# Performance work log

Measured on AMD Instinct MI355X. Metric: run time of the kernel, lower is better.

Reference implementation:

```python
import jax, jax.numpy as jnp
import numpy as np

N = 80000      # nodes
E = 1280000    # edges
G = 64         # graphs in batch
CIN = 128
D = 64
NUM_LAYERS = 6


def setup_inputs() -> dict:
    key = jax.random.key(0)
    ks = jax.random.split(key, 12)
    s = 0.05
    return {
        "x": jax.random.normal(ks[0], (N, CIN), jnp.float32),
        "edge_index": jax.random.randint(ks[1], (2, E), 0, N, dtype=jnp.int32),
        "batch": jnp.sort(jax.random.randint(ks[2], (N,), 0, G, dtype=jnp.int32)),
        "W_in": jax.random.normal(ks[3], (CIN, D), jnp.float32) * s,
        "b_in": jnp.zeros((D,), jnp.float32),
        "W_hid": jax.random.normal(ks[4], (NUM_LAYERS - 1, D, D), jnp.float32) * s,
        "b_hid": jnp.zeros((NUM_LAYERS - 1, D), jnp.float32),
        "lin1_w": jax.random.normal(ks[5], (2 * D, 64), jnp.float32) * s,
        "lin1_b": jnp.zeros((64,), jnp.float32),
        "lin2_w": jax.random.normal(ks[6], (64, 64), jnp.float32) * s,
        "lin2_b": jnp.zeros((64,), jnp.float32),
        "lin3_w": jax.random.normal(ks[7], (64, 1), jnp.float32) * s,
        "lin3_b": jnp.zeros((1,), jnp.float32),
    }


def _gcn_norm(edge_index, n):
    # PyG gcn_norm: add self-loops, symmetric D^-1/2 (A+I) D^-1/2 normalization
    loops = jnp.arange(n, dtype=edge_index.dtype)
    src = jnp.concatenate([edge_index[0], loops])
    dst = jnp.concatenate([edge_index[1], loops])
    deg = jax.ops.segment_sum(jnp.ones_like(src, jnp.float32), dst, num_segments=n)
    dinv = jnp.where(deg > 0, jax.lax.rsqrt(jnp.maximum(deg, 1.0)), 0.0)
    norm = dinv[src] * dinv[dst]
    return src, dst, norm


def _gcn_conv(x, W, b, src, dst, norm, n):
    h = x @ W                                   # [N, D]
    msg = h[src] * norm[:, None]                # [E+N, D] gather + scale
    out = jax.ops.segment_sum(msg, dst, num_segments=n)
    return out + b


def reference(x, edge_index, batch, W_in, b_in, W_hid, b_hid,
              lin1_w, lin1_b, lin2_w, lin2_b, lin3_w, lin3_b):
    n = x.shape[0]
    src, dst, norm = _gcn_norm(edge_index, n)
    # layer 0: in_channels -> D, then ReLU
    h = jax.nn.relu(_gcn_conv(x, W_in, b_in, src, dst, norm, n))
    # hidden layers: ReLU on all but the last conv
    n_hid = W_hid.shape[0]
    for i in range(n_hid):
        h = _gcn_conv(h, W_hid[i], b_hid[i], src, dst, norm, n)
        if i != n_hid - 1:
            h = jax.nn.relu(h)
    # global add + max pooling per graph
    x1 = jax.ops.segment_sum(h, batch, num_segments=G)   # [G, D]
    x2 = jax.ops.segment_max(h, batch, num_segments=G)   # [G, D]
    g = jnp.concatenate([x1, x2], axis=1)                # [G, 2D]
    g = jax.nn.relu(g @ lin1_w + lin1_b)
    g = jax.nn.relu(g @ lin2_w + lin2_b)
    return g @ lin3_w + lin3_b                           # [G, 1]
```

## Files before the change

### kernel.cpp

```cpp
#include <hip/hip_runtime.h>
#include <hip/hip_bf16.h>
#include <cstdint>
#include <cstddef>


#define FEAT 64


__global__ __launch_bounds__(256) void init_kernel(int* deg, int* cursor,
    float* gsum, unsigned int* gmax, int n) {
  int i = blockIdx.x * 256 + threadIdx.x;
  if (i < n) { deg[i] = 0; cursor[i] = 0; }
  if (i < 64 * FEAT) { gsum[i] = 0.f; gmax[i] = 0xFF800000u; }
}

__global__ __launch_bounds__(256) void hist_kernel(const int* __restrict__ dst,
    int* __restrict__ deg, int e) {
  int i = blockIdx.x * 256 + threadIdx.x;
  if (i < e) atomicAdd(&deg[dst[i]], 1);
}

__global__ __launch_bounds__(256) void dinv_kernel(const int* __restrict__ deg,
    float* __restrict__ dinv, int n) {
  int i = blockIdx.x * 256 + threadIdx.x;
  if (i < n) dinv[i] = rsqrtf((float)(deg[i] + 1));
}

__global__ __launch_bounds__(256) void scan1_kernel(const int* __restrict__ deg,
    int* __restrict__ offs, int* __restrict__ bsums, int n) {
  __shared__ int buf[256];
  int t = threadIdx.x;
  int i = blockIdx.x * 256 + t;
  int v = (i < n) ? deg[i] : 0;
  buf[t] = v;
  __syncthreads();
  for (int off = 1; off < 256; off <<= 1) {
    int add = (t >= off) ? buf[t - off] : 0;
    __syncthreads();
    buf[t] += add;
    __syncthreads();
  }
  if (i < n) offs[i] = buf[t] - v;
  if (t == 255) bsums[blockIdx.x] = buf[255];
}

__global__ __launch_bounds__(512) void scan2_kernel(int* bs, int nb) {
  __shared__ int buf[512];
  int t = threadIdx.x;
  int v = (t < nb) ? bs[t] : 0;
  buf[t] = v;
  __syncthreads();
  for (int off = 1; off < 512; off <<= 1) {
    int add = (t >= off) ? buf[t - off] : 0;
    __syncthreads();
    buf[t] += add;
    __syncthreads();
  }
  if (t < nb) bs[t] = buf[t] - v;
}

__global__ __launch_bounds__(256) void scan3_kernel(int* __restrict__ offs,
    const int* __restrict__ bs, int n) {
  int i = blockIdx.x * 256 + threadIdx.x;
  if (i < n) offs[i] += bs[blockIdx.x];
}

__global__ __launch_bounds__(256) void fill_kernel(const int* __restrict__ src,
    const int* __restrict__ dst, const int* __restrict__ offs,
    int* __restrict__ cursor, int* __restrict__ csr_src, int e) {
  int i = blockIdx.x * 256 + threadIdx.x;
  if (i >= e) return;
  int d = dst[i], s = src[i];
  int pos = offs[d] + atomicAdd(&cursor[d], 1);
  csr_src[pos] = s;
}

template <int K>
__global__ __launch_bounds__(256, 2) void gemm_kernel(
    const float* __restrict__ in, const float* __restrict__ W,
    const float* __restrict__ dinv, float* __restrict__ out, int n) {
  __shared__ float in_lds[64 * K];
  const int lane = threadIdx.x & 63;
  const int wid = threadIdx.x >> 6;

  float wreg[K];
#pragma unroll
  for (int k = 0; k < K; ++k) wreg[k] = W[k * 64 + lane];

  const int ntiles = n >> 6;
  for (int tile = blockIdx.x; tile < ntiles; tile += gridDim.x) {
    const float* tin = in + (size_t)tile * 64 * K;
    __syncthreads();
#pragma unroll
    for (int i = threadIdx.x; i < 16 * K; i += 256)
      *(float4*)&in_lds[i * 4] = *(const float4*)&tin[i * 4];
    __syncthreads();

    float* tout = out + (size_t)tile * 64 * 64;
    const float* dvp = dinv + tile * 64;
#pragma unroll
    for (int g = 0; g < 4; ++g) {
      const int r0 = wid * 16 + g * 4;
      float a0 = 0.f, a1 = 0.f, a2 = 0.f, a3 = 0.f;
#pragma unroll
      for (int k = 0; k < K; k += 4) {
        float4 x0 = *(const float4*)&in_lds[(r0 + 0) * K + k];
        float4 x1 = *(const float4*)&in_lds[(r0 + 1) * K + k];
        float4 x2 = *(const float4*)&in_lds[(r0 + 2) * K + k];
        float4 x3 = *(const float4*)&in_lds[(r0 + 3) * K + k];
        a0 = fmaf(x0.x, wreg[k + 0], a0); a0 = fmaf(x0.y, wreg[k + 1], a0);
        a0 = fmaf(x0.z, wreg[k + 2], a0); a0 = fmaf(x0.w, wreg[k + 3], a0);
        a1 = fmaf(x1.x, wreg[k + 0], a1); a1 = fmaf(x1.y, wreg[k + 1], a1);
        a1 = fmaf(x1.z, wreg[k + 2], a1); a1 = fmaf(x1.w, wreg[k + 3], a1);
        a2 = fmaf(x2.x, wreg[k + 0], a2); a2 = fmaf(x2.y, wreg[k + 1], a2);
        a2 = fmaf(x2.z, wreg[k + 2], a2); a2 = fmaf(x2.w, wreg[k + 3], a2);
        a3 = fmaf(x3.x, wreg[k + 0], a3); a3 = fmaf(x3.y, wreg[k + 1], a3);
        a3 = fmaf(x3.z, wreg[k + 2], a3); a3 = fmaf(x3.w, wreg[k + 3], a3);
      }
      tout[(r0 + 0) * 64 + lane] = a0 * dvp[r0 + 0];
      tout[(r0 + 1) * 64 + lane] = a1 * dvp[r0 + 1];
      tout[(r0 + 2) * 64 + lane] = a2 * dvp[r0 + 2];
      tout[(r0 + 3) * 64 + lane] = a3 * dvp[r0 + 3];
    }
  }
}

__global__ __launch_bounds__(256) void agg_kernel(const float* __restrict__ t,
    const int* __restrict__ csr_src, const int* __restrict__ offs,
    const int* __restrict__ cnt, const float* __restrict__ dinv,
    const float* __restrict__ bias, float* __restrict__ h, int n, int relu) {
  int wave = (blockIdx.x * 256 + threadIdx.x) >> 6;
  int lane = threadIdx.x & 63;
  if (wave >= n) return;
  int v = wave;
  float acc = t[(size_t)v * 64 + lane];
  int j = offs[v];
  int end = j + cnt[v];
  for (; j + 3 < end; j += 4) {
    int s0 = csr_src[j + 0], s1 = csr_src[j + 1];
    int s2 = csr_src[j + 2], s3 = csr_src[j + 3];
    float t0 = t[(size_t)s0 * 64 + lane];
    float t1 = t[(size_t)s1 * 64 + lane];
    float t2 = t[(size_t)s2 * 64 + lane];
    float t3 = t[(size_t)s3 * 64 + lane];
    acc += t0 + t1 + t2 + t3;
  }
  for (; j < end; ++j) {
    int s = csr_src[j];
    acc += t[(size_t)s * 64 + lane];
  }
  acc = fmaf(dinv[v], acc, bias[lane]);
  if (relu) acc = fmaxf(acc, 0.f);
  h[(size_t)v * 64 + lane] = acc;
}


__device__ inline void atomic_max_float(float* addr, float val) {
  if (val >= 0.f)
    atomicMax((int*)addr, __float_as_int(val));
  else
    atomicMin((unsigned int*)addr, (unsigned int)__float_as_int(val));
}

#define POOL_CHUNK 128

__global__ __launch_bounds__(256) void pool_kernel(const float* __restrict__ h,
    const int* __restrict__ batch, float* __restrict__ gsum,
    float* __restrict__ gmax, int n) {
  int wave = (blockIdx.x * 256 + threadIdx.x) >> 6;
  int lane = threadIdx.x & 63;
  int start = wave * POOL_CHUNK;
  if (start >= n) return;
  int end = min(start + POOL_CHUNK, n);
  float s = 0.f, m = -INFINITY;
  int cur = batch[start];
  for (int v = start; v < end; ++v) {
    int g = batch[v];
    if (g != cur) {
      atomicAdd(&gsum[cur * 64 + lane], s);
      atomic_max_float(&gmax[cur * 64 + lane], m);
      s = 0.f; m = -INFINITY; cur = g;
    }
    float x = h[(size_t)v * 64 + lane];
    s += x;
    m = fmaxf(m, x);
  }
  atomicAdd(&gsum[cur * 64 + lane], s);
  atomic_max_float(&gmax[cur * 64 + lane], m);
}


__global__ __launch_bounds__(256) void mlp_kernel(const float* __restrict__ gsum,
    const float* __restrict__ gmax, const float* __restrict__ w1,
    const float* __restrict__ b1, const float* __restrict__ w2,
    const float* __restrict__ b2, const float* __restrict__ w3,
    const float* __restrict__ b3, float* __restrict__ out) {
  __shared__ float smem[64 * 128 + 64 * 64];
  float* gg = smem;
  float* z1 = smem + 64 * 128;
  int t = threadIdx.x;
  for (int i = t; i < 64 * 128; i += 256) {
    int g = i >> 7, f = i & 127;
    gg[i] = (f < 64) ? gsum[g * 64 + f] : gmax[g * 64 + (f - 64)];
  }
  __syncthreads();
  for (int i = t; i < 64 * 64; i += 256) {
    int g = i >> 6, j = i & 63;
    float acc = b1[j];
    for (int f = 0; f < 128; ++f) acc = fmaf(gg[(g << 7) + f], w1[f * 64 + j], acc);
    z1[i] = fmaxf(acc, 0.f);
  }
  __syncthreads();
  float* z2 = smem;
  for (int i = t; i < 64 * 64; i += 256) {
    int g = i >> 6, j = i & 63;
    float acc = b2[j];
    for (int f = 0; f < 64; ++f) acc = fmaf(z1[(g << 6) + f], w2[f * 64 + j], acc);
    z2[i] = fmaxf(acc, 0.f);
  }
  __syncthreads();
  if (t < 64) {
    float acc = b3[0];
    for (int j = 0; j < 64; ++j) acc = fmaf(z2[(t << 6) + j], w3[j], acc);
    out[t] = acc;
  }
}


extern "C" void kernel_launch(void* const* d_in, const int* in_sizes, int n_in,
                              void* d_out, int out_size, void* d_ws, size_t ws_size,
                              hipStream_t stream) {
  const float* x      = (const float*)d_in[0];
  const int*   eidx   = (const int*)d_in[1];
  const int*   batch  = (const int*)d_in[2];
  const float* W_in   = (const float*)d_in[3];
  const float* b_in   = (const float*)d_in[4];
  const float* W_hid  = (const float*)d_in[5];
  const float* b_hid  = (const float*)d_in[6];
  const float* lin1_w = (const float*)d_in[7];
  const float* lin1_b = (const float*)d_in[8];
  const float* lin2_w = (const float*)d_in[9];
  const float* lin2_b = (const float*)d_in[10];
  const float* lin3_w = (const float*)d_in[11];
  const float* lin3_b = (const float*)d_in[12];
  float* out = (float*)d_out;

  const int N = in_sizes[2];
  const int E = in_sizes[1] / 2;
  const int CIN = in_sizes[0] / N;
  const int n_hid = in_sizes[5] / (64 * 64);

  const int* src = eidx;
  const int* dst = eidx + E;

  char* ws = (char*)d_ws;
  size_t off = 0;
  auto alloc = [&](size_t bytes) {
    size_t o = off;
    off = (off + bytes + 255) & ~(size_t)255;
    return o;
  };
  int*   deg     = (int*)(ws + alloc((size_t)N * 4));
  int*   cursor  = (int*)(ws + alloc((size_t)N * 4));
  float* dinv    = (float*)(ws + alloc((size_t)N * 4));
  int*   offs    = (int*)(ws + alloc((size_t)N * 4));
  int*   bsums   = (int*)(ws + alloc(1024 * 4));
  int*   csr_src = (int*)(ws + alloc((size_t)E * 4));
  float* tbuf    = (float*)(ws + alloc((size_t)N * 64 * 4));
  float* hbuf    = (float*)(ws + alloc((size_t)N * 64 * 4));
  float* gsum    = (float*)(ws + alloc(64 * 64 * 4));
  float* gmax    = (float*)(ws + alloc(64 * 64 * 4));
  (void)ws_size; (void)n_in; (void)out_size; (void)CIN;

  const int nbN = (N + 255) / 256;
  const int nbE = (E + 255) / 256;

  init_kernel<<<nbN, 256, 0, stream>>>(deg, cursor, gsum, (unsigned int*)gmax, N);
  hist_kernel<<<nbE, 256, 0, stream>>>(dst, deg, E);
  dinv_kernel<<<nbN, 256, 0, stream>>>(deg, dinv, N);
  scan1_kernel<<<nbN, 256, 0, stream>>>(deg, offs, bsums, N);
  scan2_kernel<<<1, 512, 0, stream>>>(bsums, nbN);
  scan3_kernel<<<nbN, 256, 0, stream>>>(offs, bsums, N);
  fill_kernel<<<nbE, 256, 0, stream>>>(src, dst, offs, cursor, csr_src, E);

  const int ntiles = N >> 6;
  const int agg_blocks = (N * 64 + 255) / 256;

  gemm_kernel<128><<<ntiles, 256, 0, stream>>>(x, W_in, dinv, tbuf, N);
  agg_kernel<<<agg_blocks, 256, 0, stream>>>(tbuf, csr_src, offs, deg,
                                             dinv, b_in, hbuf, N, 1);
  for (int i = 0; i < n_hid; ++i) {
    gemm_kernel<64><<<ntiles, 256, 0, stream>>>(hbuf, W_hid + (size_t)i * 64 * 64,
                                                dinv, tbuf, N);
    agg_kernel<<<agg_blocks, 256, 0, stream>>>(tbuf, csr_src, offs, deg,
                                               dinv, b_hid + (size_t)i * 64, hbuf, N,
                                               (i != n_hid - 1) ? 1 : 0);
  }

  const int pool_waves = (N + POOL_CHUNK - 1) / POOL_CHUNK;
  const int pool_blocks = (pool_waves * 64 + 255) / 256;
  pool_kernel<<<pool_blocks, 256, 0, stream>>>(hbuf, batch, gsum, gmax, N);

  mlp_kernel<<<1, 256, 0, stream>>>(gsum, gmax, lin1_w, lin1_b, lin2_w, lin2_b,
                                    lin3_w, lin3_b, out);
}
```

Measured before the change: 792.3 us.

## Store gathered messages in bf16 and slice CSR build atomics by destination range

The per-layer transformed features written by the GEMM and gathered in aggregation are now stored as bf16 instead of fp32, halving the bytes moved by the random neighbor gathers. Accumulation stays in fp32. Histogram and CSR fill kernels are also restructured so that each block handles only one eighth of the destination range, improving atomic locality at the cost of every slice rereading the edge list. This adds bf16 rounding error to messages, and the slicing assumes N is divisible by 8.

Measured after the change: 730.8 us. 7.8% less time.

```diff
diff --git a/kernel.cpp b/kernel.cpp
--- a/kernel.cpp
+++ b/kernel.cpp
@@ -5,6 +5,15 @@
 
 
 #define FEAT 64
+
+static __device__ inline unsigned short f2bf(float f) {
+  unsigned u = __float_as_uint(f);
+  unsigned r = (u + 0x7FFF + ((u >> 16) & 1)) >> 16;
+  return (unsigned short)r;
+}
+static __device__ inline float bf2f(unsigned short u) {
+  return __uint_as_float(((unsigned)u) << 16);
+}
 
 
 __global__ __launch_bounds__(256) void init_kernel(int* deg, int* cursor,
@@ -15,9 +24,16 @@
 }
 
 __global__ __launch_bounds__(256) void hist_kernel(const int* __restrict__ dst,
-    int* __restrict__ deg, int e) {
-  int i = blockIdx.x * 256 + threadIdx.x;
-  if (i < e) atomicAdd(&deg[dst[i]], 1);
+    int* __restrict__ deg, int e, int n) {
+  const int slice = blockIdx.x & 7;
+  const int lo = slice * (n >> 3);
+  const int hi = lo + (n >> 3);
+  const int nb = gridDim.x >> 3;
+  const int bid = blockIdx.x >> 3;
+  for (int i = bid * 256 + threadIdx.x; i < e; i += nb * 256) {
+    int d = dst[i];
+    if (d >= lo && d < hi) atomicAdd(&deg[d], 1);
+  }
 }
 
 __global__ __launch_bounds__(256) void dinv_kernel(const int* __restrict__ deg,
@@ -67,18 +83,25 @@
 
 __global__ __launch_bounds__(256) void fill_kernel(const int* __restrict__ src,
     const int* __restrict__ dst, const int* __restrict__ offs,
-    int* __restrict__ cursor, int* __restrict__ csr_src, int e) {
-  int i = blockIdx.x * 256 + threadIdx.x;
-  if (i >= e) return;
-  int d = dst[i], s = src[i];
-  int pos = offs[d] + atomicAdd(&cursor[d], 1);
-  csr_src[pos] = s;
+    int* __restrict__ cursor, int* __restrict__ csr_src, int e, int n) {
+  const int slice = blockIdx.x & 7;
+  const int lo = slice * (n >> 3);
+  const int hi = lo + (n >> 3);
+  const int nb = gridDim.x >> 3;
+  const int bid = blockIdx.x >> 3;
+  for (int i = bid * 256 + threadIdx.x; i < e; i += nb * 256) {
+    int d = dst[i];
+    if (d >= lo && d < hi) {
+      int pos = offs[d] + atomicAdd(&cursor[d], 1);
+      csr_src[pos] = src[i];
+    }
+  }
 }
 
 template <int K>
 __global__ __launch_bounds__(256, 2) void gemm_kernel(
     const float* __restrict__ in, const float* __restrict__ W,
-    const float* __restrict__ dinv, float* __restrict__ out, int n) {
+    const float* __restrict__ dinv, unsigned short* __restrict__ tg, int n) {
   __shared__ float in_lds[64 * K];
   const int lane = threadIdx.x & 63;
   const int wid = threadIdx.x >> 6;
@@ -96,7 +119,7 @@
       *(float4*)&in_lds[i * 4] = *(const float4*)&tin[i * 4];
     __syncthreads();
 
-    float* tout = out + (size_t)tile * 64 * 64;
+    unsigned short* tout = tg + (size_t)tile * 64 * 64;
     const float* dvp = dinv + tile * 64;
 #pragma unroll
     for (int g = 0; g < 4; ++g) {
@@ -117,37 +140,38 @@
         a3 = fmaf(x3.x, wreg[k + 0], a3); a3 = fmaf(x3.y, wreg[k + 1], a3);
         a3 = fmaf(x3.z, wreg[k + 2], a3); a3 = fmaf(x3.w, wreg[k + 3], a3);
       }
-      tout[(r0 + 0) * 64 + lane] = a0 * dvp[r0 + 0];
-      tout[(r0 + 1) * 64 + lane] = a1 * dvp[r0 + 1];
-      tout[(r0 + 2) * 64 + lane] = a2 * dvp[r0 + 2];
-      tout[(r0 + 3) * 64 + lane] = a3 * dvp[r0 + 3];
+      tout[(r0 + 0) * 64 + lane] = f2bf(a0 * dvp[r0 + 0]);
+      tout[(r0 + 1) * 64 + lane] = f2bf(a1 * dvp[r0 + 1]);
+      tout[(r0 + 2) * 64 + lane] = f2bf(a2 * dvp[r0 + 2]);
+      tout[(r0 + 3) * 64 + lane] = f2bf(a3 * dvp[r0 + 3]);
     }
   }
 }
 
-__global__ __launch_bounds__(256) void agg_kernel(const float* __restrict__ t,
-    const int* __restrict__ csr_src, const int* __restrict__ offs,
-    const int* __restrict__ cnt, const float* __restrict__ dinv,
-    const float* __restrict__ bias, float* __restrict__ h, int n, int relu) {
+__global__ __launch_bounds__(256) void agg_kernel(
+    const unsigned short* __restrict__ tg, const int* __restrict__ csr_src,
+    const int* __restrict__ offs, const int* __restrict__ cnt,
+    const float* __restrict__ dinv, const float* __restrict__ bias,
+    float* __restrict__ h, int n, int relu) {
   int wave = (blockIdx.x * 256 + threadIdx.x) >> 6;
   int lane = threadIdx.x & 63;
   if (wave >= n) return;
   int v = wave;
-  float acc = t[(size_t)v * 64 + lane];
+  float acc = bf2f(tg[(size_t)v * 64 + lane]);
   int j = offs[v];
   int end = j + cnt[v];
   for (; j + 3 < end; j += 4) {
     int s0 = csr_src[j + 0], s1 = csr_src[j + 1];
     int s2 = csr_src[j + 2], s3 = csr_src[j + 3];
-    float t0 = t[(size_t)s0 * 64 + lane];
-    float t1 = t[(size_t)s1 * 64 + lane];
-    float t2 = t[(size_t)s2 * 64 + lane];
-    float t3 = t[(size_t)s3 * 64 + lane];
-    acc += t0 + t1 + t2 + t3;
+    unsigned short u0 = tg[(size_t)s0 * 64 + lane];
+    unsigned short u1 = tg[(size_t)s1 * 64 + lane];
+    unsigned short u2 = tg[(size_t)s2 * 64 + lane];
+    unsigned short u3 = tg[(size_t)s3 * 64 + lane];
+    acc += bf2f(u0) + bf2f(u1) + bf2f(u2) + bf2f(u3);
   }
   for (; j < end; ++j) {
     int s = csr_src[j];
-    acc += t[(size_t)s * 64 + lane];
+    acc += bf2f(tg[(size_t)s * 64 + lane]);
   }
   acc = fmaf(dinv[v], acc, bias[lane]);
   if (relu) acc = fmaxf(acc, 0.f);
@@ -260,39 +284,38 @@
     off = (off + bytes + 255) & ~(size_t)255;
     return o;
   };
-  int*   deg     = (int*)(ws + alloc((size_t)N * 4));
-  int*   cursor  = (int*)(ws + alloc((size_t)N * 4));
-  float* dinv    = (float*)(ws + alloc((size_t)N * 4));
-  int*   offs    = (int*)(ws + alloc((size_t)N * 4));
-  int*   bsums   = (int*)(ws + alloc(1024 * 4));
-  int*   csr_src = (int*)(ws + alloc((size_t)E * 4));
-  float* tbuf    = (float*)(ws + alloc((size_t)N * 64 * 4));
-  float* hbuf    = (float*)(ws + alloc((size_t)N * 64 * 4));
-  float* gsum    = (float*)(ws + alloc(64 * 64 * 4));
-  float* gmax    = (float*)(ws + alloc(64 * 64 * 4));
+  int*            deg     = (int*)(ws + alloc((size_t)N * 4));
+  int*            cursor  = (int*)(ws + alloc((size_t)N * 4));
+  float*          dinv    = (float*)(ws + alloc((size_t)N * 4));
+  int*            offs    = (int*)(ws + alloc((size_t)N * 4));
+  int*            bsums   = (int*)(ws + alloc(1024 * 4));
+  int*            csr_src = (int*)(ws + alloc((size_t)E * 4));
+  unsigned short* tg      = (unsigned short*)(ws + alloc((size_t)N * 64 * 2));
+  float*          hbuf    = (float*)(ws + alloc((size_t)N * 64 * 4));
+  float*          gsum    = (float*)(ws + alloc(64 * 64 * 4));
+  float*          gmax    = (float*)(ws + alloc(64 * 64 * 4));
   (void)ws_size; (void)n_in; (void)out_size; (void)CIN;
 
   const int nbN = (N + 255) / 256;
-  const int nbE = (E + 255) / 256;
 
   init_kernel<<<nbN, 256, 0, stream>>>(deg, cursor, gsum, (unsigned int*)gmax, N);
-  hist_kernel<<<nbE, 256, 0, stream>>>(dst, deg, E);
+  hist_kernel<<<1024, 256, 0, stream>>>(dst, deg, E, N);
   dinv_kernel<<<nbN, 256, 0, stream>>>(deg, dinv, N);
   scan1_kernel<<<nbN, 256, 0, stream>>>(deg, offs, bsums, N);
   scan2_kernel<<<1, 512, 0, stream>>>(bsums, nbN);
   scan3_kernel<<<nbN, 256, 0, stream>>>(offs, bsums, N);
-  fill_kernel<<<nbE, 256, 0, stream>>>(src, dst, offs, cursor, csr_src, E);
+  fill_kernel<<<1024, 256, 0, stream>>>(src, dst, offs, cursor, csr_src, E, N);
 
   const int ntiles = N >> 6;
   const int agg_blocks = (N * 64 + 255) / 256;
 
-  gemm_kernel<128><<<ntiles, 256, 0, stream>>>(x, W_in, dinv, tbuf, N);
-  agg_kernel<<<agg_blocks, 256, 0, stream>>>(tbuf, csr_src, offs, deg,
+  gemm_kernel<128><<<ntiles, 256, 0, stream>>>(x, W_in, dinv, tg, N);
+  agg_kernel<<<agg_blocks, 256, 0, stream>>>(tg, csr_src, offs, deg,
                                              dinv, b_in, hbuf, N, 1);
   for (int i = 0; i < n_hid; ++i) {
     gemm_kernel<64><<<ntiles, 256, 0, stream>>>(hbuf, W_hid + (size_t)i * 64 * 64,
-                                                dinv, tbuf, N);
-    agg_kernel<<<agg_blocks, 256, 0, stream>>>(tbuf, csr_src, offs, deg,
+                                                dinv, tg, N);
+    agg_kernel<<<agg_blocks, 256, 0, stream>>>(tg, csr_src, offs, deg,
                                                dinv, b_hid + (size_t)i * 64, hbuf, N,
                                                (i != n_hid - 1) ? 1 : 0);
   }
```
